# Kernel optimization log

Hardware: AMD Instinct MI355X
Metric: run time of the kernel (lower is better)

## Reference

```python
import jax, jax.numpy as jnp
import numpy as np

ATOM_TYPES = [1, 6, 7, 8, 16]
GRID_LENGTHS = [8.0, 12.0]
GRID_SIZE = 16


def _make_grid(L, G):
    # vertices of the cubic grid, (G, G, G, 3), matching torch generate_grid (ij ordering)
    ticks = jnp.linspace(-L / 2.0, L / 2.0, G)
    return jnp.stack(jnp.meshgrid(ticks, ticks, ticks, indexing='ij'), axis=-1)


def reference(distance_vector, sigma, atomic_numbers):
    # distance_vector: (B, A, N, 3); atomic_numbers: (A, N); sigma: (1,)
    coeff = -0.5 / (sigma ** 2)  # (1,)
    reps = []
    for Z in ATOM_TYPES:
        mask = (atomic_numbers == Z).astype(distance_vector.dtype)  # (A, N)
        d = distance_vector * mask[None, :, :, None]                # (B, A, N, 3)
        d_sq = jnp.sum(d * d, axis=-1)                              # (B, A, N)
        for L in GRID_LENGTHS:
            grid = _make_grid(L, GRID_SIZE)                         # (G, G, G, 3)
            g_sq = jnp.sum(grid * grid, axis=-1)                    # (G, G, G)
            # ||grid - d||^2 = |grid|^2 + |d|^2 - 2 d.grid  (avoids (...,3) broadcast)
            dot = jnp.einsum('banc,xyzc->banxyz', d, grid)          # (B, A, N, G, G, G)
            sq = g_sq[None, None, None] + d_sq[..., None, None, None] - 2.0 * dot
            box = jnp.exp(coeff * sq).sum(axis=2)                   # (B, A, G, G, G)
            reps.append(box)
    return jnp.stack(reps, axis=2)  # (B, A, C, G, G, G)


def setup_inputs() -> dict:
    key = jax.random.key(0)
    k1, k2 = jax.random.split(key)
    distance_vector = jax.random.normal(k1, (1, 128, 64, 3), dtype=jnp.float32) * 3.0
    atomic_numbers = jax.random.randint(k2, (128, 64), 0, 17).astype(jnp.int64)
    sigma = jnp.ones((1,), dtype=jnp.float32)
    return {'distance_vector': distance_vector, 'sigma': sigma, 'atomic_numbers': atomic_numbers}
```

## Files before the change

### kernel.cpp

```cpp
#include <hip/hip_runtime.h>

static constexpr int kA = 128;
static constexpr int kN = 64;
static constexpr int kG = 16;
static constexpr int kC = 10;
static constexpr int kS = 17;


__global__ __launch_bounds__(256) void voxel_kernel(
    const float* __restrict__ dvec,
    const float* __restrict__ sigma,
    const int*   __restrict__ zn,
    float*       __restrict__ out)
{
    const int blk = blockIdx.x;
    const int a   = blk / 10;
    const int c   = blk - a * 10;
    const int ch  = c >> 1;
    const int li  = c & 1;

    const int Ztab[5] = {1, 6, 7, 8, 16};
    const int Ztarget = Ztab[ch];

    const float Lg   = li ? 12.0f : 8.0f;
    const float step = Lg * (1.0f / 15.0f);
    const float t0   = -0.5f * Lg;
    const float sg   = sigma[0];
    const float coeff = -0.5f / (sg * sg);

    const int t = threadIdx.x;

    __shared__ float s_tab[3 * kN * kS];
    __shared__ float s_e0[kG];

    if (t < 192) {
        const int ax = t >> 6;
        const int n  = t & 63;
        const float d = dvec[(size_t)a * (kN * 3) + n * 3 + ax];
        float* dst = &s_tab[(ax * kN + n) * kS];
#pragma unroll
        for (int i = 0; i < kG; ++i) {
            const float r = (t0 + i * step) - d;
            dst[i] = __expf(coeff * r * r);
        }
    } else if (t < 192 + kG) {
        const int i = t - 192;
        const float r = t0 + i * step;
        s_e0[i] = __expf(coeff * r * r);
    }

    const int lane = t & 63;
    const int Zl   = zn[a * kN + lane];
    unsigned long long mask = __ballot(Zl == Ztarget);
    const int cnt = __popcll(mask);

    __syncthreads();

    const int y  = (t >> 2) & 15;
    const int zq = (t & 3) * 4;
    const int xb = t >> 6;

    const float* s_ex = &s_tab[0 * kN * kS];
    const float* s_ey = &s_tab[1 * kN * kS];
    const float* s_ez = &s_tab[2 * kN * kS];

    float acc[4][4];
    {
        const float w  = (float)(kN - cnt) * s_e0[y];
        float ez0[4];
#pragma unroll
        for (int j = 0; j < 4; ++j) ez0[j] = s_e0[zq + j];
#pragma unroll
        for (int i = 0; i < 4; ++i) {
            const float wx = w * s_e0[xb + 4 * i];
#pragma unroll
            for (int j = 0; j < 4; ++j)
                acc[i][j] = wx * ez0[j];
        }
    }

    while (mask) {
        const int n = (int)__builtin_ctzll(mask);
        mask &= mask - 1ull;
        const int nS = n * kS;
        const float eyn = s_ey[nS + y];
        float ezn[4];
#pragma unroll
        for (int j = 0; j < 4; ++j) ezn[j] = s_ez[nS + zq + j];
#pragma unroll
        for (int i = 0; i < 4; ++i) {
            const float p = s_ex[nS + xb + 4 * i] * eyn;
#pragma unroll
            for (int j = 0; j < 4; ++j)
                acc[i][j] = fmaf(p, ezn[j], acc[i][j]);
        }
    }

    float4* o = (float4*)(out + ((size_t)a * kC + c) * (kG * kG * kG));
#pragma unroll
    for (int q = 0; q < 4; ++q)
        o[t + 256 * q] = make_float4(acc[q][0], acc[q][1], acc[q][2], acc[q][3]);
}

extern "C" void kernel_launch(void* const* d_in, const int* in_sizes, int n_in,
                              void* d_out, int out_size, void* d_ws, size_t ws_size,
                              hipStream_t stream) {
    const float* dvec  = (const float*)d_in[0];
    const float* sigma = (const float*)d_in[1];
    const int*   zn    = (const int*)d_in[2];
    float* out = (float*)d_out;

    voxel_kernel<<<dim3(kA * kC), dim3(256), 0, stream>>>(dvec, sigma, zn, out);
}
```

Before: 66.11 us.

## Share per-atom gaussian tables across all five atom-type channels per block

Each block now handles one atom-molecule and one grid length for all five atom-type channels, instead of one channel per block. The 1D exponential tables are built once and reused across channels, which removes five-fold redundant exp computation and table setup. Blocks grow to 512 threads with 2x4 outputs per thread, and the grid shrinks from 1280 to 256 blocks. With only 256 blocks on a GPU with many CUs, occupancy may be low and the per-block serial work is longer.

```diff
diff --git a/kernel.cpp b/kernel.cpp
--- a/kernel.cpp
+++ b/kernel.cpp
@@ -7,20 +7,15 @@
 static constexpr int kS = 17;
 
 
-__global__ __launch_bounds__(256) void voxel_kernel(
+__global__ __launch_bounds__(512) void voxel_kernel(
     const float* __restrict__ dvec,
     const float* __restrict__ sigma,
     const int*   __restrict__ zn,
     float*       __restrict__ out)
 {
     const int blk = blockIdx.x;
-    const int a   = blk / 10;
-    const int c   = blk - a * 10;
-    const int ch  = c >> 1;
-    const int li  = c & 1;
-
-    const int Ztab[5] = {1, 6, 7, 8, 16};
-    const int Ztarget = Ztab[ch];
+    const int a   = blk >> 1;
+    const int li  = blk & 1;
 
     const float Lg   = li ? 12.0f : 8.0f;
     const float step = Lg * (1.0f / 15.0f);
@@ -51,8 +46,14 @@
 
     const int lane = t & 63;
     const int Zl   = zn[a * kN + lane];
-    unsigned long long mask = __ballot(Zl == Ztarget);
-    const int cnt = __popcll(mask);
+    const int Ztab[5] = {1, 6, 7, 8, 16};
+    unsigned long long masks[5];
+    int cnts[5];
+#pragma unroll
+    for (int ch = 0; ch < 5; ++ch) {
+        masks[ch] = __ballot(Zl == Ztab[ch]);
+        cnts[ch]  = __popcll(masks[ch]);
+    }
 
     __syncthreads();
 
@@ -64,42 +65,50 @@
     const float* s_ey = &s_tab[1 * kN * kS];
     const float* s_ez = &s_tab[2 * kN * kS];
 
-    float acc[4][4];
-    {
-        const float w  = (float)(kN - cnt) * s_e0[y];
-        float ez0[4];
+    const float e0y = s_e0[y];
+    float e0x[2];
+    e0x[0] = s_e0[xb];
+    e0x[1] = s_e0[xb + 8];
+    float ez0[4];
 #pragma unroll
-        for (int j = 0; j < 4; ++j) ez0[j] = s_e0[zq + j];
+    for (int j = 0; j < 4; ++j) ez0[j] = s_e0[zq + j];
+
 #pragma unroll
-        for (int i = 0; i < 4; ++i) {
-            const float wx = w * s_e0[xb + 4 * i];
+    for (int ch = 0; ch < 5; ++ch) {
+        float acc[2][4];
+        const float w = (float)(kN - cnts[ch]) * e0y;
+#pragma unroll
+        for (int i = 0; i < 2; ++i) {
+            const float wx = w * e0x[i];
 #pragma unroll
             for (int j = 0; j < 4; ++j)
                 acc[i][j] = wx * ez0[j];
         }
+
+        unsigned long long mask = masks[ch];
+        while (mask) {
+            const int n = (int)__builtin_ctzll(mask);
+            mask &= mask - 1ull;
+            const int nS = n * kS;
+            const float eyn = s_ey[nS + y];
+            float ezn[4];
+#pragma unroll
+            for (int j = 0; j < 4; ++j) ezn[j] = s_ez[nS + zq + j];
+#pragma unroll
+            for (int i = 0; i < 2; ++i) {
+                const float p = s_ex[nS + xb + 8 * i] * eyn;
+#pragma unroll
+                for (int j = 0; j < 4; ++j)
+                    acc[i][j] = fmaf(p, ezn[j], acc[i][j]);
+            }
+        }
+
+        const int c = ch * 2 + li;
+        float4* o = (float4*)(out + ((size_t)a * kC + c) * (kG * kG * kG));
+#pragma unroll
+        for (int q = 0; q < 2; ++q)
+            o[t + 512 * q] = make_float4(acc[q][0], acc[q][1], acc[q][2], acc[q][3]);
     }
-
-    while (mask) {
-        const int n = (int)__builtin_ctzll(mask);
-        mask &= mask - 1ull;
-        const int nS = n * kS;
-        const float eyn = s_ey[nS + y];
-        float ezn[4];
-#pragma unroll
-        for (int j = 0; j < 4; ++j) ezn[j] = s_ez[nS + zq + j];
-#pragma unroll
-        for (int i = 0; i < 4; ++i) {
-            const float p = s_ex[nS + xb + 4 * i] * eyn;
-#pragma unroll
-            for (int j = 0; j < 4; ++j)
-                acc[i][j] = fmaf(p, ezn[j], acc[i][j]);
-        }
-    }
-
-    float4* o = (float4*)(out + ((size_t)a * kC + c) * (kG * kG * kG));
-#pragma unroll
-    for (int q = 0; q < 4; ++q)
-        o[t + 256 * q] = make_float4(acc[q][0], acc[q][1], acc[q][2], acc[q][3]);
 }
 
 extern "C" void kernel_launch(void* const* d_in, const int* in_sizes, int n_in,
@@ -110,5 +119,5 @@
     const int*   zn    = (const int*)d_in[2];
     float* out = (float*)d_out;
 
-    voxel_kernel<<<dim3(kA * kC), dim3(256), 0, stream>>>(dvec, sigma, zn, out);
+    voxel_kernel<<<dim3(kA * 2), dim3(512), 0, stream>>>(dvec, sigma, zn, out);
 }
```

Result: no change. 65.85 us (-0.4%).
